# Kernel tuning notes

Hardware: AMD Instinct MI355X
Metric: run time of the kernel (lower is better)

Reference implementation:

```python
import jax, jax.numpy as jnp
import numpy as np

MODES1 = 32
MODES2 = 32


def _dct1_last(x):
    # Unnormalized DCT-I along last axis via rfft of even-symmetric extension.
    # For length N input, extension [x0..x_{N-1}, x_{N-2}..x_1] has length 2(N-1);
    # rfft yields N real coefficients == scipy.fftpack.dct(x, type=1).
    ext = jnp.concatenate([x, x[..., -2:0:-1]], axis=-1)
    return jnp.fft.rfft(ext, axis=-1).real.astype(x.dtype)


def _dct1_2d(x):
    # DCT-I along last two axes (separable). scipy idct type-1 (unnormalized)
    # is identical to dct type-1, so this serves as both dctn and idctn.
    x = _dct1_last(x)
    x = jnp.swapaxes(x, -1, -2)
    x = _dct1_last(x)
    return jnp.swapaxes(x, -1, -2)


def setup_inputs() -> dict:
    key = jax.random.key(0)
    k1, k2, k3 = jax.random.split(key, 3)
    B, Cin, Cout, H, W = 8, 64, 64, 256, 256
    scale = 1.0 / (Cin * Cout)
    x = jax.random.normal(k1, (B, Cin, H, W), dtype=jnp.float32)
    weights1 = scale * jax.random.uniform(k2, (Cin, Cout, MODES1, MODES2), dtype=jnp.float32)
    weights2 = scale * jax.random.uniform(k3, (Cin, Cout, MODES1, MODES2), dtype=jnp.float32)
    return {"x": x, "weights1": weights1, "weights2": weights2}


def reference(x, weights1, weights2):
    B, Cin, H, W = x.shape
    Cout = weights1.shape[1]
    Wh = W // 2 + 1  # width of truncated spectral tensor (torch used cfloat, imag==0)
    m1, m2 = MODES1, MODES2

    x_dct = _dct1_2d(x)  # [B, Cin, H, W]

    low = jnp.einsum('bixy,ioxy->boxy', x_dct[:, :, :m1, :m2], weights1)
    high = jnp.einsum('bixy,ioxy->boxy', x_dct[:, :, -m1:, :m2], weights2)

    out_ft = jnp.zeros((B, Cout, H, Wh), dtype=x.dtype)
    out_ft = out_ft.at[:, :, :m1, :m2].set(low)
    out_ft = out_ft.at[:, :, H - m1:, :m2].set(high)

    # idctn(..., type=1, shape=(H, W)) zero-pads the last axis from Wh to W,
    # then applies unnormalized IDCT-I == DCT-I along axes 2,3.
    out_full = jnp.pad(out_ft, ((0, 0), (0, 0), (0, 0), (0, W - Wh)))
    return _dct1_2d(out_full)
```

## Files before the change

kernel.cpp:

```cpp
#include <hip/hip_runtime.h>
#include <math.h>

#define OFF_AT  0
#define OFF_BMT 16384
#define OFF_CMT 24576
#define OFF_DMT 40960
#define OFF_Y   49152
#define OFF_Z   1097728

__device__ __forceinline__ float cosT(int p) {
    int r = p % 510;
    if (r > 255) r = 510 - r;
    return cosf((float)r * (3.14159265358979323846f / 255.0f));
}

__global__ __launch_bounds__(256) void init_basis(float* __restrict__ ws) {
    int idx = blockIdx.x * 256 + threadIdx.x;
    if (idx < 16384) {
        int h = idx >> 6, r = idx & 63;
        int k1 = (r < 32) ? r : r + 192;
        float we = (h == 0 || h == 255) ? 1.f : 2.f;
        ws[OFF_AT + idx] = we * cosT(k1 * h);
    } else if (idx < 24576) {
        int j = idx - 16384; int w = j >> 5, y = j & 31;
        float we = (w == 0 || w == 255) ? 1.f : 2.f;
        ws[OFF_BMT + j] = we * cosT(y * w);
    } else if (idx < 40960) {
        int j = idx - 24576; int r = j >> 8, h = j & 255;
        int k1 = (r < 32) ? r : r + 192;
        float wsl = (r == 0 || r == 63) ? 1.f : 2.f;
        ws[OFF_CMT + j] = wsl * cosT(k1 * h);
    } else if (idx < 49152) {
        int j = idx - 40960; int y = j >> 8, w = j & 255;
        float wy = (y == 0) ? 1.f : 2.f;
        ws[OFF_DMT + j] = wy * cosT(y * w);
    }
}

__global__ __launch_bounds__(256) void fwd_kernel(const float* __restrict__ x,
                                                  const float* __restrict__ ws,
                                                  float* __restrict__ Y) {
    __shared__ float buf[9216];
    __shared__ float bmt[1024];
    const int t = threadIdx.x;
    const int bi = blockIdx.x;
    const float* xp = x + (size_t)bi * 65536;
    const int l = t & 63;
    const int y8 = (t >> 6) * 8;

    float acc[4][8];
#pragma unroll
    for (int j = 0; j < 4; ++j)
#pragma unroll
        for (int yy = 0; yy < 8; ++yy) acc[j][yy] = 0.f;

    const int colv = (t & 7) * 4;
    const int rbase = t >> 3;

    for (int c = 0; c < 8; ++c) {
#pragma unroll
        for (int r = 0; r < 8; ++r) {
            int row = r * 32 + rbase;
            float4 v = *(const float4*)(xp + row * 256 + c * 32 + colv);
            float* dst = &buf[row * 33 + colv];
            dst[0] = v.x; dst[1] = v.y; dst[2] = v.z; dst[3] = v.w;
        }
        {
            int wloc = t >> 3;
            int y4 = (t & 7) * 4;
            *(float4*)&bmt[wloc * 32 + y4] =
                *(const float4*)(ws + OFF_BMT + (c * 32 + wloc) * 32 + y4);
        }
        __syncthreads();
#pragma unroll 8
        for (int w = 0; w < 32; ++w) {
            float xv0 = buf[l * 33 + w];
            float xv1 = buf[(l + 64) * 33 + w];
            float xv2 = buf[(l + 128) * 33 + w];
            float xv3 = buf[(l + 192) * 33 + w];
            float4 b0 = *(float4*)&bmt[w * 32 + y8];
            float4 b1 = *(float4*)&bmt[w * 32 + y8 + 4];
            float bv[8] = {b0.x, b0.y, b0.z, b0.w, b1.x, b1.y, b1.z, b1.w};
#pragma unroll
            for (int yy = 0; yy < 8; ++yy) {
                acc[0][yy] += xv0 * bv[yy];
                acc[1][yy] += xv1 * bv[yy];
                acc[2][yy] += xv2 * bv[yy];
                acc[3][yy] += xv3 * bv[yy];
            }
        }
        __syncthreads();
    }
#pragma unroll
    for (int j = 0; j < 4; ++j)
#pragma unroll
        for (int yy = 0; yy < 8; ++yy)
            buf[(l + 64 * j) * 36 + y8 + yy] = acc[j][yy];
    __syncthreads();

    float acc2[8];
#pragma unroll
    for (int yy = 0; yy < 8; ++yy) acc2[yy] = 0.f;
    const float* At = ws + OFF_AT;
#pragma unroll 4
    for (int h = 0; h < 256; ++h) {
        float av = At[h * 64 + l];
        float4 t0 = *(float4*)&buf[h * 36 + y8];
        float4 t1 = *(float4*)&buf[h * 36 + y8 + 4];
        acc2[0] += av * t0.x; acc2[1] += av * t0.y;
        acc2[2] += av * t0.z; acc2[3] += av * t0.w;
        acc2[4] += av * t1.x; acc2[5] += av * t1.y;
        acc2[6] += av * t1.z; acc2[7] += av * t1.w;
    }
    float* Yp = Y + (size_t)bi * 2048 + l * 32 + y8;
    *(float4*)Yp       = make_float4(acc2[0], acc2[1], acc2[2], acc2[3]);
    *(float4*)(Yp + 4) = make_float4(acc2[4], acc2[5], acc2[6], acc2[7]);
}

__global__ __launch_bounds__(256) void mix_kernel(const float* __restrict__ w1,
                                                  const float* __restrict__ w2,
                                                  const float* __restrict__ Yv,
                                                  float* __restrict__ Z) {
    const int xp = blockIdx.x & 63;
    const int o0 = (blockIdx.x >> 6) * 16;
    const int t = threadIdx.x;
    const int yh = t & 15;
    const int oo = t >> 4;
    const int o = o0 + oo;
    const int y = yh * 2;

    const float* Wbase = (xp < 32) ? (w1 + xp * 32) : (w2 + (xp - 32) * 32);
    Wbase += o * 1024 + y;
    const float* Yb = Yv + xp * 32 + y;

    float acc[8][2];
#pragma unroll
    for (int b = 0; b < 8; ++b) { acc[b][0] = 0.f; acc[b][1] = 0.f; }

    for (int i = 0; i < 64; ++i) {
        float2 wv = *(const float2*)(Wbase + i * 65536);
#pragma unroll
        for (int b = 0; b < 8; ++b) {
            float2 yv = *(const float2*)(Yb + (b * 64 + i) * 2048);
            acc[b][0] += yv.x * wv.x;
            acc[b][1] += yv.y * wv.y;
        }
    }
#pragma unroll
    for (int b = 0; b < 8; ++b) {
        float2 r; r.x = acc[b][0]; r.y = acc[b][1];
        *(float2*)(Z + (size_t)(b * 64 + o) * 2048 + xp * 32 + y) = r;
    }
}

__global__ __launch_bounds__(256) void inv_kernel(const float* __restrict__ ws,
                                                  const float* __restrict__ Zv,
                                                  float* __restrict__ out) {
    __shared__ float zs[2048];
    __shared__ float dmts[8192];
    __shared__ float t2t[4224];
    const int t = threadIdx.x;
    const int bo = blockIdx.x;
    const float* Zp = Zv + (size_t)bo * 2048;
    float* op = out + (size_t)bo * 65536;

    *(float4*)&zs[t * 8]     = *(const float4*)(Zp + t * 8);
    *(float4*)&zs[t * 8 + 4] = *(const float4*)(Zp + t * 8 + 4);
#pragma unroll
    for (int k = 0; k < 8; ++k)
        *(float4*)&dmts[k * 1024 + t * 4] =
            *(const float4*)(ws + OFF_DMT + k * 1024 + t * 4);
    __syncthreads();

    const int l6 = t & 63;
    const int y8 = (t >> 6) * 8;
    const int l5 = t & 31;
    const int j  = t >> 5;

    for (int hh = 0; hh < 2; ++hh) {
        float a1[2][8];
#pragma unroll
        for (int jj = 0; jj < 2; ++jj)
#pragma unroll
            for (int yy = 0; yy < 8; ++yy) a1[jj][yy] = 0.f;
        const float* Cm = ws + OFF_CMT + hh * 128 + l6;
#pragma unroll 4
        for (int xpi = 0; xpi < 64; ++xpi) {
            float av0 = Cm[xpi * 256];
            float av1 = Cm[xpi * 256 + 64];
            float4 z0 = *(float4*)&zs[xpi * 32 + y8];
            float4 z1 = *(float4*)&zs[xpi * 32 + y8 + 4];
            float zv[8] = {z0.x, z0.y, z0.z, z0.w, z1.x, z1.y, z1.z, z1.w};
#pragma unroll
            for (int yy = 0; yy < 8; ++yy) {
                a1[0][yy] += av0 * zv[yy];
                a1[1][yy] += av1 * zv[yy];
            }
        }
#pragma unroll
        for (int jj = 0; jj < 2; ++jj)
#pragma unroll
            for (int yy = 0; yy < 8; ++yy)
                t2t[(y8 + yy) * 132 + l6 + 64 * jj] = a1[jj][yy];
        __syncthreads();

        for (int hg = 0; hg < 2; ++hg) {
            float a2[8][8];
#pragma unroll
            for (int ii = 0; ii < 8; ++ii)
#pragma unroll
                for (int ww = 0; ww < 8; ++ww) a2[ii][ww] = 0.f;
            const int hb = hg * 64 + j * 8;
#pragma unroll 4
            for (int y = 0; y < 32; ++y) {
                float4 ta = *(float4*)&t2t[y * 132 + hb];
                float4 tb = *(float4*)&t2t[y * 132 + hb + 4];
                float4 da = *(float4*)&dmts[y * 256 + l5 * 8];
                float4 db = *(float4*)&dmts[y * 256 + l5 * 8 + 4];
                float tv[8] = {ta.x, ta.y, ta.z, ta.w, tb.x, tb.y, tb.z, tb.w};
                float dv[8] = {da.x, da.y, da.z, da.w, db.x, db.y, db.z, db.w};
#pragma unroll
                for (int ii = 0; ii < 8; ++ii)
#pragma unroll
                    for (int ww = 0; ww < 8; ++ww)
                        a2[ii][ww] += tv[ii] * dv[ww];
            }
#pragma unroll
            for (int ii = 0; ii < 8; ++ii) {
                int h = hh * 128 + hb + ii;
                float* o8 = op + h * 256 + l5 * 8;
                *(float4*)o8       = make_float4(a2[ii][0], a2[ii][1], a2[ii][2], a2[ii][3]);
                *(float4*)(o8 + 4) = make_float4(a2[ii][4], a2[ii][5], a2[ii][6], a2[ii][7]);
            }
        }
        __syncthreads();
    }
}

extern "C" void kernel_launch(void* const* d_in, const int* in_sizes, int n_in,
                              void* d_out, int out_size, void* d_ws, size_t ws_size,
                              hipStream_t stream) {
    const float* x  = (const float*)d_in[0];
    const float* w1 = (const float*)d_in[1];
    const float* w2 = (const float*)d_in[2];
    float* out = (float*)d_out;
    float* ws  = (float*)d_ws;

    hipLaunchKernelGGL(init_basis, dim3(192), dim3(256), 0, stream, ws);
    hipLaunchKernelGGL(fwd_kernel, dim3(512), dim3(256), 0, stream, x, ws, ws + OFF_Y);
    hipLaunchKernelGGL(mix_kernel, dim3(256), dim3(256), 0, stream, w1, w2,
                       ws + OFF_Y, ws + OFF_Z);
    hipLaunchKernelGGL(inv_kernel, dim3(512), dim3(256), 0, stream, ws, ws + OFF_Z, out);
}
```

Before: 326.3 us.

## Split forward and inverse transform kernels into two stages via global intermediates

Splits the fused forward kernel into a row-transform kernel (two blocks per image) and a column-contraction kernel, and the inverse kernel into two kernels with 2x and 4x more blocks. Intermediate results go through global workspace instead of shared memory. The aim is more blocks, less shared memory and fewer registers per block, so occupancy and spread across CUs improve. In exchange it adds extra global traffic for the intermediates and two more kernel launches.

Measured after the change: 347.9 us. +6.6%, slower.

```diff
diff --git a/kernel.cpp b/kernel.cpp
--- a/kernel.cpp
+++ b/kernel.cpp
@@ -5,8 +5,9 @@
 #define OFF_BMT 16384
 #define OFF_CMT 24576
 #define OFF_DMT 40960
-#define OFF_Y   49152
-#define OFF_Z   1097728
+#define OFF_T   49152
+#define OFF_Y   4243456
+#define OFF_Z   5292032
 
 __device__ __forceinline__ float cosT(int p) {
     int r = p % 510;
@@ -37,84 +38,92 @@
     }
 }
 
-__global__ __launch_bounds__(256) void fwd_kernel(const float* __restrict__ x,
-                                                  const float* __restrict__ ws,
-                                                  float* __restrict__ Y) {
-    __shared__ float buf[9216];
-    __shared__ float bmt[1024];
-    const int t = threadIdx.x;
-    const int bi = blockIdx.x;
-    const float* xp = x + (size_t)bi * 65536;
+__global__ __launch_bounds__(256) void fwd1_kernel(const float* __restrict__ x,
+                                                   const float* __restrict__ ws,
+                                                   float* __restrict__ T1) {
+    __shared__ float xs[128 * 33];
+    __shared__ float bs[32 * 32];
+    const int t = threadIdx.x;
+    const int bi = blockIdx.x >> 1;
+    const int rt = (blockIdx.x & 1) * 128;
+    const float* xp = x + (size_t)bi * 65536 + (size_t)rt * 256;
     const int l = t & 63;
     const int y8 = (t >> 6) * 8;
-
-    float acc[4][8];
-#pragma unroll
-    for (int j = 0; j < 4; ++j)
-#pragma unroll
-        for (int yy = 0; yy < 8; ++yy) acc[j][yy] = 0.f;
-
     const int colv = (t & 7) * 4;
     const int rbase = t >> 3;
 
+    float acc0[8], acc1[8];
+#pragma unroll
+    for (int yy = 0; yy < 8; ++yy) { acc0[yy] = 0.f; acc1[yy] = 0.f; }
+
     for (int c = 0; c < 8; ++c) {
 #pragma unroll
-        for (int r = 0; r < 8; ++r) {
+        for (int r = 0; r < 4; ++r) {
             int row = r * 32 + rbase;
             float4 v = *(const float4*)(xp + row * 256 + c * 32 + colv);
-            float* dst = &buf[row * 33 + colv];
+            float* dst = &xs[row * 33 + colv];
             dst[0] = v.x; dst[1] = v.y; dst[2] = v.z; dst[3] = v.w;
         }
         {
             int wloc = t >> 3;
             int y4 = (t & 7) * 4;
-            *(float4*)&bmt[wloc * 32 + y4] =
+            *(float4*)&bs[wloc * 32 + y4] =
                 *(const float4*)(ws + OFF_BMT + (c * 32 + wloc) * 32 + y4);
         }
         __syncthreads();
 #pragma unroll 8
         for (int w = 0; w < 32; ++w) {
-            float xv0 = buf[l * 33 + w];
-            float xv1 = buf[(l + 64) * 33 + w];
-            float xv2 = buf[(l + 128) * 33 + w];
-            float xv3 = buf[(l + 192) * 33 + w];
-            float4 b0 = *(float4*)&bmt[w * 32 + y8];
-            float4 b1 = *(float4*)&bmt[w * 32 + y8 + 4];
+            float xv0 = xs[l * 33 + w];
+            float xv1 = xs[(l + 64) * 33 + w];
+            float4 b0 = *(float4*)&bs[w * 32 + y8];
+            float4 b1 = *(float4*)&bs[w * 32 + y8 + 4];
             float bv[8] = {b0.x, b0.y, b0.z, b0.w, b1.x, b1.y, b1.z, b1.w};
 #pragma unroll
             for (int yy = 0; yy < 8; ++yy) {
-                acc[0][yy] += xv0 * bv[yy];
-                acc[1][yy] += xv1 * bv[yy];
-                acc[2][yy] += xv2 * bv[yy];
-                acc[3][yy] += xv3 * bv[yy];
+                acc0[yy] += xv0 * bv[yy];
+                acc1[yy] += xv1 * bv[yy];
             }
         }
         __syncthreads();
     }
-#pragma unroll
-    for (int j = 0; j < 4; ++j)
-#pragma unroll
-        for (int yy = 0; yy < 8; ++yy)
-            buf[(l + 64 * j) * 36 + y8 + yy] = acc[j][yy];
+    float* Tp = T1 + (size_t)bi * 8192 + (size_t)(rt + l) * 32 + y8;
+    *(float4*)Tp       = make_float4(acc0[0], acc0[1], acc0[2], acc0[3]);
+    *(float4*)(Tp + 4) = make_float4(acc0[4], acc0[5], acc0[6], acc0[7]);
+    Tp += 64 * 32;
+    *(float4*)Tp       = make_float4(acc1[0], acc1[1], acc1[2], acc1[3]);
+    *(float4*)(Tp + 4) = make_float4(acc1[4], acc1[5], acc1[6], acc1[7]);
+}
+
+__global__ __launch_bounds__(256) void fwd2_kernel(const float* __restrict__ ws,
+                                                   const float* __restrict__ T1,
+                                                   float* __restrict__ Y) {
+    __shared__ float t1s[8192];
+    const int t = threadIdx.x;
+    const int bi = blockIdx.x;
+    const float* Tp = T1 + (size_t)bi * 8192;
+#pragma unroll
+    for (int k = 0; k < 8; ++k)
+        *(float4*)&t1s[k * 1024 + t * 4] = *(const float4*)(Tp + k * 1024 + t * 4);
     __syncthreads();
-
-    float acc2[8];
-#pragma unroll
-    for (int yy = 0; yy < 8; ++yy) acc2[yy] = 0.f;
-    const float* At = ws + OFF_AT;
+    const int l = t & 63;
+    const int y8 = (t >> 6) * 8;
+    float acc[8];
+#pragma unroll
+    for (int yy = 0; yy < 8; ++yy) acc[yy] = 0.f;
+    const float* At = ws + OFF_AT + l;
 #pragma unroll 4
     for (int h = 0; h < 256; ++h) {
-        float av = At[h * 64 + l];
-        float4 t0 = *(float4*)&buf[h * 36 + y8];
-        float4 t1 = *(float4*)&buf[h * 36 + y8 + 4];
-        acc2[0] += av * t0.x; acc2[1] += av * t0.y;
-        acc2[2] += av * t0.z; acc2[3] += av * t0.w;
-        acc2[4] += av * t1.x; acc2[5] += av * t1.y;
-        acc2[6] += av * t1.z; acc2[7] += av * t1.w;
+        float av = At[h * 64];
+        float4 t0 = *(float4*)&t1s[h * 32 + y8];
+        float4 t1v = *(float4*)&t1s[h * 32 + y8 + 4];
+        acc[0] += av * t0.x;  acc[1] += av * t0.y;
+        acc[2] += av * t0.z;  acc[3] += av * t0.w;
+        acc[4] += av * t1v.x; acc[5] += av * t1v.y;
+        acc[6] += av * t1v.z; acc[7] += av * t1v.w;
     }
     float* Yp = Y + (size_t)bi * 2048 + l * 32 + y8;
-    *(float4*)Yp       = make_float4(acc2[0], acc2[1], acc2[2], acc2[3]);
-    *(float4*)(Yp + 4) = make_float4(acc2[4], acc2[5], acc2[6], acc2[7]);
+    *(float4*)Yp       = make_float4(acc[0], acc[1], acc[2], acc[3]);
+    *(float4*)(Yp + 4) = make_float4(acc[4], acc[5], acc[6], acc[7]);
 }
 
 __global__ __launch_bounds__(256) void mix_kernel(const float* __restrict__ w1,
@@ -153,87 +162,86 @@
     }
 }
 
-__global__ __launch_bounds__(256) void inv_kernel(const float* __restrict__ ws,
-                                                  const float* __restrict__ Zv,
-                                                  float* __restrict__ out) {
+__global__ __launch_bounds__(256) void inv1_kernel(const float* __restrict__ ws,
+                                                   const float* __restrict__ Zv,
+                                                   float* __restrict__ T2) {
     __shared__ float zs[2048];
-    __shared__ float dmts[8192];
-    __shared__ float t2t[4224];
-    const int t = threadIdx.x;
-    const int bo = blockIdx.x;
+    const int t = threadIdx.x;
+    const int bo = blockIdx.x >> 1;
+    const int ht = (blockIdx.x & 1) * 128;
     const float* Zp = Zv + (size_t)bo * 2048;
-    float* op = out + (size_t)bo * 65536;
-
     *(float4*)&zs[t * 8]     = *(const float4*)(Zp + t * 8);
     *(float4*)&zs[t * 8 + 4] = *(const float4*)(Zp + t * 8 + 4);
-#pragma unroll
-    for (int k = 0; k < 8; ++k)
-        *(float4*)&dmts[k * 1024 + t * 4] =
-            *(const float4*)(ws + OFF_DMT + k * 1024 + t * 4);
     __syncthreads();
-
-    const int l6 = t & 63;
+    const int l = t & 63;
     const int y8 = (t >> 6) * 8;
-    const int l5 = t & 31;
-    const int j  = t >> 5;
-
-    for (int hh = 0; hh < 2; ++hh) {
-        float a1[2][8];
-#pragma unroll
-        for (int jj = 0; jj < 2; ++jj)
-#pragma unroll
-            for (int yy = 0; yy < 8; ++yy) a1[jj][yy] = 0.f;
-        const float* Cm = ws + OFF_CMT + hh * 128 + l6;
+    float acc0[8], acc1[8];
+#pragma unroll
+    for (int yy = 0; yy < 8; ++yy) { acc0[yy] = 0.f; acc1[yy] = 0.f; }
+    const float* Cm = ws + OFF_CMT + ht + l;
 #pragma unroll 4
-        for (int xpi = 0; xpi < 64; ++xpi) {
-            float av0 = Cm[xpi * 256];
-            float av1 = Cm[xpi * 256 + 64];
-            float4 z0 = *(float4*)&zs[xpi * 32 + y8];
-            float4 z1 = *(float4*)&zs[xpi * 32 + y8 + 4];
-            float zv[8] = {z0.x, z0.y, z0.z, z0.w, z1.x, z1.y, z1.z, z1.w};
-#pragma unroll
-            for (int yy = 0; yy < 8; ++yy) {
-                a1[0][yy] += av0 * zv[yy];
-                a1[1][yy] += av1 * zv[yy];
-            }
-        }
-#pragma unroll
-        for (int jj = 0; jj < 2; ++jj)
-#pragma unroll
-            for (int yy = 0; yy < 8; ++yy)
-                t2t[(y8 + yy) * 132 + l6 + 64 * jj] = a1[jj][yy];
-        __syncthreads();
-
-        for (int hg = 0; hg < 2; ++hg) {
-            float a2[8][8];
-#pragma unroll
-            for (int ii = 0; ii < 8; ++ii)
-#pragma unroll
-                for (int ww = 0; ww < 8; ++ww) a2[ii][ww] = 0.f;
-            const int hb = hg * 64 + j * 8;
+    for (int r = 0; r < 64; ++r) {
+        float a0 = Cm[r * 256];
+        float a1 = Cm[r * 256 + 64];
+        float4 z0 = *(float4*)&zs[r * 32 + y8];
+        float4 z1 = *(float4*)&zs[r * 32 + y8 + 4];
+        float zv[8] = {z0.x, z0.y, z0.z, z0.w, z1.x, z1.y, z1.z, z1.w};
+#pragma unroll
+        for (int yy = 0; yy < 8; ++yy) {
+            acc0[yy] += a0 * zv[yy];
+            acc1[yy] += a1 * zv[yy];
+        }
+    }
+    float* Tp = T2 + (size_t)bo * 8192 + (size_t)y8 * 256 + ht + l;
+#pragma unroll
+    for (int j = 0; j < 8; ++j) {
+        Tp[j * 256]      = acc0[j];
+        Tp[j * 256 + 64] = acc1[j];
+    }
+}
+
+__global__ __launch_bounds__(256) void inv2_kernel(const float* __restrict__ ws,
+                                                   const float* __restrict__ T2,
+                                                   float* __restrict__ out) {
+    __shared__ float t2s[32 * 68];
+    const int t = threadIdx.x;
+    const int bo = blockIdx.x >> 2;
+    const int ht = (blockIdx.x & 3) * 64;
+    const float* Tp = T2 + (size_t)bo * 8192 + ht;
+    {
+        int y = t >> 3;
+        int c8 = (t & 7) * 8;
+        *(float4*)&t2s[y * 68 + c8]     = *(const float4*)(Tp + y * 256 + c8);
+        *(float4*)&t2s[y * 68 + c8 + 4] = *(const float4*)(Tp + y * 256 + c8 + 4);
+    }
+    __syncthreads();
+    const int h8 = (t >> 5) * 8;
+    const int w8 = (t & 31) * 8;
+    const float* Dm = ws + OFF_DMT + w8;
+    float a2[8][8];
+#pragma unroll
+    for (int i = 0; i < 8; ++i)
+#pragma unroll
+        for (int w = 0; w < 8; ++w) a2[i][w] = 0.f;
 #pragma unroll 4
-            for (int y = 0; y < 32; ++y) {
-                float4 ta = *(float4*)&t2t[y * 132 + hb];
-                float4 tb = *(float4*)&t2t[y * 132 + hb + 4];
-                float4 da = *(float4*)&dmts[y * 256 + l5 * 8];
-                float4 db = *(float4*)&dmts[y * 256 + l5 * 8 + 4];
-                float tv[8] = {ta.x, ta.y, ta.z, ta.w, tb.x, tb.y, tb.z, tb.w};
-                float dv[8] = {da.x, da.y, da.z, da.w, db.x, db.y, db.z, db.w};
-#pragma unroll
-                for (int ii = 0; ii < 8; ++ii)
-#pragma unroll
-                    for (int ww = 0; ww < 8; ++ww)
-                        a2[ii][ww] += tv[ii] * dv[ww];
-            }
-#pragma unroll
-            for (int ii = 0; ii < 8; ++ii) {
-                int h = hh * 128 + hb + ii;
-                float* o8 = op + h * 256 + l5 * 8;
-                *(float4*)o8       = make_float4(a2[ii][0], a2[ii][1], a2[ii][2], a2[ii][3]);
-                *(float4*)(o8 + 4) = make_float4(a2[ii][4], a2[ii][5], a2[ii][6], a2[ii][7]);
-            }
-        }
-        __syncthreads();
+    for (int y = 0; y < 32; ++y) {
+        float4 ta = *(float4*)&t2s[y * 68 + h8];
+        float4 tb = *(float4*)&t2s[y * 68 + h8 + 4];
+        float4 da = *(const float4*)(Dm + y * 256);
+        float4 db = *(const float4*)(Dm + y * 256 + 4);
+        float tv[8] = {ta.x, ta.y, ta.z, ta.w, tb.x, tb.y, tb.z, tb.w};
+        float dv[8] = {da.x, da.y, da.z, da.w, db.x, db.y, db.z, db.w};
+#pragma unroll
+        for (int i = 0; i < 8; ++i)
+#pragma unroll
+            for (int w = 0; w < 8; ++w)
+                a2[i][w] += tv[i] * dv[w];
+    }
+    float* op = out + (size_t)bo * 65536 + (size_t)(ht + h8) * 256 + w8;
+#pragma unroll
+    for (int i = 0; i < 8; ++i) {
+        *(float4*)(op + i * 256)     = make_float4(a2[i][0], a2[i][1], a2[i][2], a2[i][3]);
+        *(float4*)(op + i * 256 + 4) = make_float4(a2[i][4], a2[i][5], a2[i][6], a2[i][7]);
     }
 }
 
@@ -247,8 +255,10 @@
     float* ws  = (float*)d_ws;
 
     hipLaunchKernelGGL(init_basis, dim3(192), dim3(256), 0, stream, ws);
-    hipLaunchKernelGGL(fwd_kernel, dim3(512), dim3(256), 0, stream, x, ws, ws + OFF_Y);
+    hipLaunchKernelGGL(fwd1_kernel, dim3(1024), dim3(256), 0, stream, x, ws, ws + OFF_T);
+    hipLaunchKernelGGL(fwd2_kernel, dim3(512), dim3(256), 0, stream, ws, ws + OFF_T, ws + OFF_Y);
     hipLaunchKernelGGL(mix_kernel, dim3(256), dim3(256), 0, stream, w1, w2,
                        ws + OFF_Y, ws + OFF_Z);
-    hipLaunchKernelGGL(inv_kernel, dim3(512), dim3(256), 0, stream, ws, ws + OFF_Z, out);
-}
+    hipLaunchKernelGGL(inv1_kernel, dim3(1024), dim3(256), 0, stream, ws, ws + OFF_Z, ws + OFF_T);
+    hipLaunchKernelGGL(inv2_kernel, dim3(2048), dim3(256), 0, stream, ws, ws + OFF_T, out);
+}
```
